# Optimization experiments

Measured on AMD Instinct MI355X. Metric: run time of the kernel, lower is better.

## Reference

```python
import jax, jax.numpy as jnp
import numpy as np

KH = KW = 3
STRIDE = 1
PAD = 1
DIL = 1


def setup_inputs() -> dict:
    key = jax.random.key(0)
    k1, k2, k3, k4 = jax.random.split(key, 4)
    B, C, H, W = 16, 64, 64, 64
    Cout = 64
    K = KH * KW
    x = jax.random.normal(k1, (B, C, H, W), jnp.float32)
    offset = jax.random.normal(k2, (B, 2 * K, H, W), jnp.float32)
    mask = jax.random.uniform(k3, (B, K, H, W), jnp.float32)
    # uniform(-stdv, stdv) init with stdv = 1/sqrt(C*KH*KW) ~ 0.0417; scaled normal is close enough
    weight = jax.random.normal(k4, (Cout, C, KH, KW), jnp.float32) * 0.04
    bias = jnp.zeros((Cout,), jnp.float32)  # no_bias=True -> frozen zeros, still added
    return dict(input=x, offset=offset, mask=mask, weight=weight, bias=bias)


def _bilinear(img, py, px):
    # img: [C, H, W]; py, px: [K, Ho, Wo] float sampling coords
    # DCNv2 semantics: out-of-bounds corner contributions are zero.
    H, W = img.shape[1], img.shape[2]
    y0f = jnp.floor(py)
    x0f = jnp.floor(px)
    wy = py - y0f
    wx = px - x0f
    y0 = y0f.astype(jnp.int32)
    x0 = x0f.astype(jnp.int32)
    out = jnp.zeros((img.shape[0],) + py.shape, img.dtype)
    for dy in (0, 1):
        for dx in (0, 1):
            yi = y0 + dy
            xi = x0 + dx
            valid = ((yi >= 0) & (yi < H) & (xi >= 0) & (xi < W)).astype(img.dtype)
            v = img[:, jnp.clip(yi, 0, H - 1), jnp.clip(xi, 0, W - 1)]  # [C,K,Ho,Wo]
            w = (wy if dy else 1.0 - wy) * (wx if dx else 1.0 - wx)
            out = out + v * (w * valid)[None]
    return out  # [C, K, Ho, Wo]


def reference(input, offset, mask, weight, bias):
    B, C, H, W = input.shape
    Cout, _, kh, kw = weight.shape
    K = kh * kw
    Ho = (H + 2 * PAD - (DIL * (kh - 1) + 1)) // STRIDE + 1
    Wo = (W + 2 * PAD - (DIL * (kw - 1) + 1)) // STRIDE + 1
    off = offset.reshape(B, K, 2, Ho, Wo)  # per kernel point: (dy, dx)
    ky = jnp.repeat(jnp.arange(kh), kw)  # [K] kernel row index
    kx = jnp.tile(jnp.arange(kw), kh)    # [K] kernel col index
    base_y = jnp.arange(Ho) * STRIDE - PAD
    base_x = jnp.arange(Wo) * STRIDE - PAD
    py = off[:, :, 0] + (base_y[None, None, :, None] + (ky * DIL)[None, :, None, None])
    px = off[:, :, 1] + (base_x[None, None, None, :] + (kx * DIL)[None, :, None, None])
    sampled = jax.vmap(_bilinear)(input, py, px)        # [B, C, K, Ho, Wo]
    modulated = sampled * mask[:, None]                 # mask-modulated accumulation
    out = jnp.einsum('bckpq,ock->bopq', modulated, weight.reshape(Cout, C, K))
    return out + bias[None, :, None, None]
```

## Files before the change

### kernel.cpp

```cpp
#include <hip/hip_runtime.h>

#define BATCH 16
#define C_IN  64
#define HH    64
#define WW    64
#define COUT  64
#define KK    9
#define HW    4096
#define CK    576
#define MROW  200

typedef __bf16 bf16x8 __attribute__((ext_vector_type(8)));
typedef float  f32x4  __attribute__((ext_vector_type(4)));
typedef unsigned int u32x2 __attribute__((ext_vector_type(2)));

__device__ __forceinline__ unsigned int f32_to_bf16_rne(float f) {
    unsigned int b = __float_as_uint(f);
    b += 0x7FFFu + ((b >> 16) & 1u);
    return b >> 16;
}

__global__ __launch_bounds__(256) void prep_kernel(
    const float* __restrict__ x, const float* __restrict__ w,
    unsigned short* __restrict__ xt, unsigned short* __restrict__ wt) {
    __shared__ unsigned short tile[64][72];
    const int t = threadIdx.x;
    const int blk = blockIdx.x;
    if (blk < 1024) {
        const int b = blk >> 6, y = blk & 63;
        const float* xrow = x + ((b * 64) * 64 + y) * 64;
#pragma unroll
        for (int it = 0; it < 4; ++it) {
            const int idx = it * 256 + t;
            const int c = idx >> 4, seg = idx & 15;
            const float4 v = *(const float4*)(xrow + c * HW + seg * 4);
            tile[seg * 4 + 0][c] = (unsigned short)f32_to_bf16_rne(v.x);
            tile[seg * 4 + 1][c] = (unsigned short)f32_to_bf16_rne(v.y);
            tile[seg * 4 + 2][c] = (unsigned short)f32_to_bf16_rne(v.z);
            tile[seg * 4 + 3][c] = (unsigned short)f32_to_bf16_rne(v.w);
        }
        __syncthreads();
#pragma unroll
        for (int it = 0; it < 2; ++it) {
            const int idx = it * 256 + t;
            const int xx = idx >> 3, cs = idx & 7;
            *(int4*)&xt[((b * HW) + y * 64 + xx) * 64 + cs * 8] =
                *(const int4*)&tile[xx][cs * 8];
        }
    } else {
        const int i = (blk - 1024) * 256 + t;
        const int j = i & 7;
        const int l = (i >> 3) & 63;
        const int ot = (i >> 9) & 3;
        const int r = i >> 11;
        const int ks = r % 6, kc = r / 6;
        const int o  = ot * 16 + (l & 15);
        const int kk = ks * 32 + (l >> 4) * 8 + j;
        const int tap = kk >> 6, c = kk & 63;
        const int k = kc * 3 + tap;
        wt[i] = (unsigned short)f32_to_bf16_rne(w[o * CK + c * KK + k]);
    }
}

__global__ __launch_bounds__(128, 3) void dcn_main_kernel(
    const float* __restrict__ offset, const float* __restrict__ mask,
    const unsigned short* __restrict__ xt, const unsigned short* __restrict__ wt,
    const float* __restrict__ bias, float* __restrict__ out) {
    __shared__ __align__(16) unsigned short Mlds[2][16 * MROW];
    __shared__ __align__(16) int PWw[2][144 * 4];
    __shared__ __align__(8) unsigned short PWa[2][144 * 4];

    const int t    = threadIdx.x;
    const int wave = __builtin_amdgcn_readfirstlane(t >> 6);
    const int lane = t & 63;
    const int quad = lane >> 4, m16 = lane & 15;

    const int blk = blockIdx.x;
    const int xcd = blk & 7;
    const int i8  = blk >> 3;
    const int s   = ((i8 & 31) << 3) | (i8 >> 5);
    const int b   = (xcd << 1) | (s >> 7);
    const int rr  = s & 127;
    const int row = rr >> 1;
    const int qbase = (rr & 1) * 32 + wave * 16;

    f32x4 acc[4];
#pragma unroll
    for (int ot = 0; ot < 4; ++ot)
#pragma unroll
        for (int r = 0; r < 4; ++r) acc[ot][r] = 0.f;

    const float* offb = offset + b * (2 * KK * HW) + row * 64;
    const float* mb   = mask + b * (KK * HW) + row * 64;
    const char* xtb   = (const char*)(xt + b * (HW * 64));
    char* MW = (char*)Mlds[wave];
    const int co = m16 * 8;

#pragma unroll
    for (int p = 0; p < 3; ++p) {
        if (lane < 48) {
            const int t3  = lane >> 4;
            const int tap = p * 3 + t3;
            const int pxi = lane & 15;
            const int q = qbase + pxi;
            const float oy = __builtin_nontemporal_load(&offb[(2 * tap) * HW + q]);
            const float ox = __builtin_nontemporal_load(&offb[(2 * tap + 1) * HW + q]);
            const float mk = __builtin_nontemporal_load(&mb[tap * HW + q]);
            const float py  = oy + (float)(row - 1 + p);
            const float pxf = ox + (float)(q - 1 + t3);
            const float y0f = floorf(py), x0f = floorf(pxf);
            const float wy = py - y0f, wx = pxf - x0f;
            const int y0 = (int)y0f, x0 = (int)x0f;
            const int y1 = y0 + 1,   x1 = x0 + 1;
            const float vy0 = (y0 >= 0 && y0 < HH) ? 1.f : 0.f;
            const float vy1 = (y1 >= 0 && y1 < HH) ? 1.f : 0.f;
            const float vx0 = (x0 >= 0 && x0 < WW) ? 1.f : 0.f;
            const float vx1 = (x1 >= 0 && x1 < WW) ? 1.f : 0.f;
            const float w00 = (1.f - wy) * (1.f - wx) * vy0 * vx0 * mk;
            const float w01 = (1.f - wy) * wx         * vy0 * vx1 * mk;
            const float w10 = wy * (1.f - wx)         * vy1 * vx0 * mk;
            const float w11 = wy * wx                 * vy1 * vx1 * mk;
            const int cy0 = min(max(y0, 0), HH - 1), cy1 = min(max(y1, 0), HH - 1);
            const int cx0 = min(max(x0, 0), WW - 1), cx1 = min(max(x1, 0), WW - 1);
            const int it = tap * 16 + pxi;
            int4 P0;
            P0.x = __float_as_int(w00); P0.y = __float_as_int(w01);
            P0.z = __float_as_int(w10); P0.w = __float_as_int(w11);
            *(int4*)&PWw[wave][it * 4] = P0;
            ushort4 A;
            A.x = (unsigned short)(cy0 * 64 + cx0);
            A.y = (unsigned short)(cy0 * 64 + cx1);
            A.z = (unsigned short)(cy1 * 64 + cx0);
            A.w = (unsigned short)(cy1 * 64 + cx1);
            *(ushort4*)&PWa[wave][it * 4] = A;
        }
    }

    u32x2 g[12][4];

    auto bload = [&](int kc) {
        const unsigned short* Pa = &PWa[wave][0] + 48 * kc * 4;
#pragma unroll
        for (int i = 0; i < 12; ++i) {
            const int l = i * 4 + quad;
            const ushort4 a = *(const ushort4*)(Pa + l * 4);
            g[i][0] = __builtin_nontemporal_load(
                (const u32x2*)(xtb + ((int)a.x << 7) + co));
            g[i][1] = __builtin_nontemporal_load(
                (const u32x2*)(xtb + ((int)a.y << 7) + co));
            g[i][2] = __builtin_nontemporal_load(
                (const u32x2*)(xtb + ((int)a.z << 7) + co));
            g[i][3] = __builtin_nontemporal_load(
                (const u32x2*)(xtb + ((int)a.w << 7) + co));
        }
    };

    auto bfinish = [&](int kc) {
        const int* Pw = &PWw[wave][0] + 48 * kc * 4;
#pragma unroll
        for (int i = 0; i < 12; ++i) {
            const int l = i * 4 + quad;
            const int4 p0 = *(const int4*)(Pw + l * 4);
            const float fw00 = __int_as_float(p0.x), fw01 = __int_as_float(p0.y);
            const float fw10 = __int_as_float(p0.z), fw11 = __int_as_float(p0.w);
            const u32x2 u0 = g[i][0], u1 = g[i][1], u2 = g[i][2], u3 = g[i][3];
            float v0, v1, v2, v3;
            v0 = fw00 * __uint_as_float(u0.x << 16);
            v1 = fw00 * __uint_as_float(u0.x & 0xFFFF0000u);
            v2 = fw00 * __uint_as_float(u0.y << 16);
            v3 = fw00 * __uint_as_float(u0.y & 0xFFFF0000u);
            v0 = fmaf(fw01, __uint_as_float(u1.x << 16), v0);
            v1 = fmaf(fw01, __uint_as_float(u1.x & 0xFFFF0000u), v1);
            v2 = fmaf(fw01, __uint_as_float(u1.y << 16), v2);
            v3 = fmaf(fw01, __uint_as_float(u1.y & 0xFFFF0000u), v3);
            v0 = fmaf(fw10, __uint_as_float(u2.x << 16), v0);
            v1 = fmaf(fw10, __uint_as_float(u2.x & 0xFFFF0000u), v1);
            v2 = fmaf(fw10, __uint_as_float(u2.y << 16), v2);
            v3 = fmaf(fw10, __uint_as_float(u2.y & 0xFFFF0000u), v3);
            v0 = fmaf(fw11, __uint_as_float(u3.x << 16), v0);
            v1 = fmaf(fw11, __uint_as_float(u3.x & 0xFFFF0000u), v1);
            v2 = fmaf(fw11, __uint_as_float(u3.y << 16), v2);
            v3 = fmaf(fw11, __uint_as_float(u3.y & 0xFFFF0000u), v3);
            uint2 pk;
            pk.x = (f32_to_bf16_rne(v1) << 16) | f32_to_bf16_rne(v0);
            pk.y = (f32_to_bf16_rne(v3) << 16) | f32_to_bf16_rne(v2);
            *(uint2*)(MW + (l & 15) * 400 + (l >> 4) * 128 + m16 * 8) = pk;
        }
    };

    auto phaseC = [&](int kc) {
        const unsigned short* wkc = wt + kc * (6 * 4 * 512);
#pragma unroll
        for (int ks = 0; ks < 6; ++ks) {
            const bf16x8 bfrag =
                *(const bf16x8*)(MW + m16 * 400 + ks * 64 + quad * 16);
#pragma unroll
            for (int ot = 0; ot < 4; ++ot) {
                const bf16x8 afrag =
                    *(const bf16x8*)(wkc + (ks * 4 + ot) * 512 + lane * 8);
                acc[ot] = __builtin_amdgcn_mfma_f32_16x16x32_bf16(afrag, bfrag,
                                                                  acc[ot], 0, 0, 0);
            }
        }
    };

    bload(0);
    __builtin_amdgcn_sched_barrier(0);
    for (int kc = 0; kc < 3; ++kc) {
        bfinish(kc);
        if (kc < 2) {
            bload(kc + 1);
            __builtin_amdgcn_sched_barrier(0);
        }
        phaseC(kc);
    }

    float* ob = out + b * (COUT * HW) + row * 64 + qbase + m16;
#pragma unroll
    for (int ot = 0; ot < 4; ++ot)
#pragma unroll
        for (int r = 0; r < 4; ++r) {
            const int o = ot * 16 + quad * 4 + r;
            ob[o * HW] = acc[ot][r] + bias[o];
        }
}

extern "C" void kernel_launch(void* const* d_in, const int* in_sizes, int n_in,
                              void* d_out, int out_size, void* d_ws,
                              size_t ws_size, hipStream_t stream) {
    const float* x    = (const float*)d_in[0];
    const float* off  = (const float*)d_in[1];
    const float* mask = (const float*)d_in[2];
    const float* w    = (const float*)d_in[3];
    const float* bias = (const float*)d_in[4];
    float* out = (float*)d_out;

    unsigned short* xt = (unsigned short*)d_ws;
    unsigned short* wt = (unsigned short*)((char*)d_ws + 8388608);

    prep_kernel<<<1024 + 144, 256, 0, stream>>>(x, w, xt, wt);
    dcn_main_kernel<<<2048, 128, 0, stream>>>(off, mask, xt, wt, bias, out);
}
```

Before: 120.3 us.

## Switch DCN main kernel to 32x32x16 MFMA with 32-pixel wave tiles

Each wave now covers 32 output pixels instead of 16 and uses 32x32x16 bf16 MFMA with two output tiles instead of four 16x16x32 tiles. The weight prepack layout, the LDS sample-matrix layout and the grid are changed to match. The gather loads lose their nontemporal hint, and the software prefetch of the next chunk's gathers is replaced by sequential load/finish halves. The aim is to halve weight fragment reloads per pixel and use the larger MFMA, at the cost of lower occupancy (launch bounds 3 to 2), half as many blocks, and less overlap of gather latency.

```diff
diff --git a/kernel.cpp b/kernel.cpp
--- a/kernel.cpp
+++ b/kernel.cpp
@@ -8,10 +8,10 @@
 #define KK    9
 #define HW    4096
 #define CK    576
-#define MROW  200
+#define MROWB 400
 
 typedef __bf16 bf16x8 __attribute__((ext_vector_type(8)));
-typedef float  f32x4  __attribute__((ext_vector_type(4)));
+typedef float  f32x16 __attribute__((ext_vector_type(16)));
 typedef unsigned int u32x2 __attribute__((ext_vector_type(2)));
 
 __device__ __forceinline__ unsigned int f32_to_bf16_rne(float f) {
@@ -22,7 +22,7 @@
 
 __global__ __launch_bounds__(256) void prep_kernel(
     const float* __restrict__ x, const float* __restrict__ w,
-    unsigned short* __restrict__ xt, unsigned short* __restrict__ wt) {
+    unsigned short* __restrict__ xt, unsigned short* __restrict__ wt2) {
     __shared__ unsigned short tile[64][72];
     const int t = threadIdx.x;
     const int blk = blockIdx.x;
@@ -51,44 +51,44 @@
         const int i = (blk - 1024) * 256 + t;
         const int j = i & 7;
         const int l = (i >> 3) & 63;
-        const int ot = (i >> 9) & 3;
-        const int r = i >> 11;
-        const int ks = r % 6, kc = r / 6;
-        const int o  = ot * 16 + (l & 15);
-        const int kk = ks * 32 + (l >> 4) * 8 + j;
-        const int tap = kk >> 6, c = kk & 63;
+        const int ot = (i >> 9) & 1;
+        const int r = i >> 10;
+        const int ks = r % 12, kc = r / 12;
+        const int o  = ot * 32 + (l & 31);
+        const int kl = ks * 16 + (l >> 5) * 8 + j;
+        const int tap = kl >> 6, c = kl & 63;
         const int k = kc * 3 + tap;
-        wt[i] = (unsigned short)f32_to_bf16_rne(w[o * CK + c * KK + k]);
+        wt2[i] = (unsigned short)f32_to_bf16_rne(w[o * CK + c * KK + k]);
     }
 }
 
-__global__ __launch_bounds__(128, 3) void dcn_main_kernel(
+__global__ __launch_bounds__(128, 2) void dcn_main_kernel(
     const float* __restrict__ offset, const float* __restrict__ mask,
-    const unsigned short* __restrict__ xt, const unsigned short* __restrict__ wt,
+    const unsigned short* __restrict__ xt, const unsigned short* __restrict__ wt2,
     const float* __restrict__ bias, float* __restrict__ out) {
-    __shared__ __align__(16) unsigned short Mlds[2][16 * MROW];
-    __shared__ __align__(16) int PWw[2][144 * 4];
-    __shared__ __align__(8) unsigned short PWa[2][144 * 4];
+    __shared__ __align__(16) unsigned short Mlds[2][32 * (MROWB / 2)];
+    __shared__ __align__(16) int PWw[2][288 * 4];
+    __shared__ __align__(8) unsigned short PWa[2][288 * 4];
 
     const int t    = threadIdx.x;
     const int wave = __builtin_amdgcn_readfirstlane(t >> 6);
     const int lane = t & 63;
     const int quad = lane >> 4, m16 = lane & 15;
+    const int n32  = lane & 31, half = lane >> 5;
 
     const int blk = blockIdx.x;
     const int xcd = blk & 7;
     const int i8  = blk >> 3;
-    const int s   = ((i8 & 31) << 3) | (i8 >> 5);
-    const int b   = (xcd << 1) | (s >> 7);
-    const int rr  = s & 127;
-    const int row = rr >> 1;
-    const int qbase = (rr & 1) * 32 + wave * 16;
-
-    f32x4 acc[4];
-#pragma unroll
-    for (int ot = 0; ot < 4; ++ot)
-#pragma unroll
-        for (int r = 0; r < 4; ++r) acc[ot][r] = 0.f;
+    const int s   = ((i8 & 31) << 2) | (i8 >> 5);
+    const int b   = (xcd << 1) | (s >> 6);
+    const int row = s & 63;
+    const int qb  = wave * 32;
+
+    f32x16 acc[2];
+#pragma unroll
+    for (int ot = 0; ot < 2; ++ot)
+#pragma unroll
+        for (int r = 0; r < 16; ++r) acc[ot][r] = 0.f;
 
     const float* offb = offset + b * (2 * KK * HW) + row * 64;
     const float* mb   = mask + b * (KK * HW) + row * 64;
@@ -97,17 +97,18 @@
     const int co = m16 * 8;
 
 #pragma unroll
-    for (int p = 0; p < 3; ++p) {
-        if (lane < 48) {
-            const int t3  = lane >> 4;
-            const int tap = p * 3 + t3;
-            const int pxi = lane & 15;
-            const int q = qbase + pxi;
+    for (int it = 0; it < 5; ++it) {
+        const int item = it * 64 + lane;
+        if (item < 288) {
+            const int tap = item >> 5;
+            const int pxi = item & 31;
+            const int ky = tap / 3, kx = tap - ky * 3;
+            const int q = qb + pxi;
             const float oy = __builtin_nontemporal_load(&offb[(2 * tap) * HW + q]);
             const float ox = __builtin_nontemporal_load(&offb[(2 * tap + 1) * HW + q]);
             const float mk = __builtin_nontemporal_load(&mb[tap * HW + q]);
-            const float py  = oy + (float)(row - 1 + p);
-            const float pxf = ox + (float)(q - 1 + t3);
+            const float py  = oy + (float)(row - 1 + ky);
+            const float pxf = ox + (float)(q - 1 + kx);
             const float y0f = floorf(py), x0f = floorf(pxf);
             const float wy = py - y0f, wx = pxf - x0f;
             const int y0 = (int)y0f, x0 = (int)x0f;
@@ -122,44 +123,40 @@
             const float w11 = wy * wx                 * vy1 * vx1 * mk;
             const int cy0 = min(max(y0, 0), HH - 1), cy1 = min(max(y1, 0), HH - 1);
             const int cx0 = min(max(x0, 0), WW - 1), cx1 = min(max(x1, 0), WW - 1);
-            const int it = tap * 16 + pxi;
             int4 P0;
             P0.x = __float_as_int(w00); P0.y = __float_as_int(w01);
             P0.z = __float_as_int(w10); P0.w = __float_as_int(w11);
-            *(int4*)&PWw[wave][it * 4] = P0;
+            *(int4*)&PWw[wave][item * 4] = P0;
             ushort4 A;
             A.x = (unsigned short)(cy0 * 64 + cx0);
             A.y = (unsigned short)(cy0 * 64 + cx1);
             A.z = (unsigned short)(cy1 * 64 + cx0);
             A.w = (unsigned short)(cy1 * 64 + cx1);
-            *(ushort4*)&PWa[wave][it * 4] = A;
+            *(ushort4*)&PWa[wave][item * 4] = A;
         }
     }
 
     u32x2 g[12][4];
 
-    auto bload = [&](int kc) {
-        const unsigned short* Pa = &PWa[wave][0] + 48 * kc * 4;
+    auto bload = [&](int kc, int h) {
+        const unsigned short* Pa = &PWa[wave][0] + (kc * 96 + h * 48) * 4;
 #pragma unroll
         for (int i = 0; i < 12; ++i) {
             const int l = i * 4 + quad;
             const ushort4 a = *(const ushort4*)(Pa + l * 4);
-            g[i][0] = __builtin_nontemporal_load(
-                (const u32x2*)(xtb + ((int)a.x << 7) + co));
-            g[i][1] = __builtin_nontemporal_load(
-                (const u32x2*)(xtb + ((int)a.y << 7) + co));
-            g[i][2] = __builtin_nontemporal_load(
-                (const u32x2*)(xtb + ((int)a.z << 7) + co));
-            g[i][3] = __builtin_nontemporal_load(
-                (const u32x2*)(xtb + ((int)a.w << 7) + co));
+            g[i][0] = *(const u32x2*)(xtb + ((int)a.x << 7) + co);
+            g[i][1] = *(const u32x2*)(xtb + ((int)a.y << 7) + co);
+            g[i][2] = *(const u32x2*)(xtb + ((int)a.z << 7) + co);
+            g[i][3] = *(const u32x2*)(xtb + ((int)a.w << 7) + co);
         }
     };
 
-    auto bfinish = [&](int kc) {
-        const int* Pw = &PWw[wave][0] + 48 * kc * 4;
+    auto bfinish = [&](int kc, int h) {
+        const int* Pw = &PWw[wave][0] + (kc * 96 + h * 48) * 4;
 #pragma unroll
         for (int i = 0; i < 12; ++i) {
             const int l = i * 4 + quad;
+            const int item = h * 48 + l;
             const int4 p0 = *(const int4*)(Pw + l * 4);
             const float fw00 = __int_as_float(p0.x), fw01 = __int_as_float(p0.y);
             const float fw10 = __int_as_float(p0.z), fw11 = __int_as_float(p0.w);
@@ -184,43 +181,39 @@
             uint2 pk;
             pk.x = (f32_to_bf16_rne(v1) << 16) | f32_to_bf16_rne(v0);
             pk.y = (f32_to_bf16_rne(v3) << 16) | f32_to_bf16_rne(v2);
-            *(uint2*)(MW + (l & 15) * 400 + (l >> 4) * 128 + m16 * 8) = pk;
+            *(uint2*)(MW + (item & 31) * MROWB + (item >> 5) * 128 + m16 * 8) = pk;
         }
     };
 
     auto phaseC = [&](int kc) {
-        const unsigned short* wkc = wt + kc * (6 * 4 * 512);
-#pragma unroll
-        for (int ks = 0; ks < 6; ++ks) {
+#pragma unroll
+        for (int ks = 0; ks < 12; ++ks) {
             const bf16x8 bfrag =
-                *(const bf16x8*)(MW + m16 * 400 + ks * 64 + quad * 16);
-#pragma unroll
-            for (int ot = 0; ot < 4; ++ot) {
-                const bf16x8 afrag =
-                    *(const bf16x8*)(wkc + (ks * 4 + ot) * 512 + lane * 8);
-                acc[ot] = __builtin_amdgcn_mfma_f32_16x16x32_bf16(afrag, bfrag,
+                *(const bf16x8*)(MW + n32 * MROWB + ks * 32 + half * 16);
+#pragma unroll
+            for (int ot = 0; ot < 2; ++ot) {
+                const bf16x8 afrag = *(const bf16x8*)(
+                    wt2 + (((kc * 12 + ks) * 2 + ot) << 9) + lane * 8);
+                acc[ot] = __builtin_amdgcn_mfma_f32_32x32x16_bf16(afrag, bfrag,
                                                                   acc[ot], 0, 0, 0);
             }
         }
     };
 
-    bload(0);
-    __builtin_amdgcn_sched_barrier(0);
     for (int kc = 0; kc < 3; ++kc) {
-        bfinish(kc);
-        if (kc < 2) {
-            bload(kc + 1);
-            __builtin_amdgcn_sched_barrier(0);
-        }
+        bload(kc, 0);
+        bfinish(kc, 0);
+        bload(kc, 1);
+        bfinish(kc, 1);
         phaseC(kc);
     }
 
-    float* ob = out + b * (COUT * HW) + row * 64 + qbase + m16;
-#pragma unroll
-    for (int ot = 0; ot < 4; ++ot)
-#pragma unroll
-        for (int r = 0; r < 4; ++r) {
-            const int o = ot * 16 + quad * 4 + r;
+    float* ob = out + b * (COUT * HW) + row * 64 + qb + n32;
+#pragma unroll
+    for (int ot = 0; ot < 2; ++ot)
+#pragma unroll
+        for (int r = 0; r < 16; ++r) {
+            const int o = ot * 32 + (r & 3) + 8 * (r >> 2) + 4 * half;
             ob[o * HW] = acc[ot][r] + bias[o];
         }
 }
@@ -235,9 +228,9 @@
     const float* bias = (const float*)d_in[4];
     float* out = (float*)d_out;
 
-    unsigned short* xt = (unsigned short*)d_ws;
-    unsigned short* wt = (unsigned short*)((char*)d_ws + 8388608);
-
-    prep_kernel<<<1024 + 144, 256, 0, stream>>>(x, w, xt, wt);
-    dcn_main_kernel<<<2048, 128, 0, stream>>>(off, mask, xt, wt, bias, out);
-}
+    unsigned short* xt  = (unsigned short*)d_ws;
+    unsigned short* wt2 = (unsigned short*)((char*)d_ws + 8388608);
+
+    prep_kernel<<<1024 + 144, 256, 0, stream>>>(x, w, xt, wt2);
+    dcn_main_kernel<<<1024, 128, 0, stream>>>(off, mask, xt, wt2, bias, out);
+}
```

New measurement: 113.7 us. 1.06x faster.
